# Performance work log

Hardware: AMD Instinct MI355X
Metric: run time of the kernel (lower is better)

The kernel has to match this reference:

```python
import jax, jax.numpy as jnp
import numpy as np

DOWNSAMPLE = 512  # points per cloud, from init_kwargs


def _pairwise_dist(x, y):
    """Batched Euclidean distance matrix. x: (B,n,D), y: (B,m,D) -> (B,n,m)."""
    x2 = jnp.sum(x * x, axis=-1)                     # (B,n)
    y2 = jnp.sum(y * y, axis=-1)                     # (B,m)
    d2 = x2[:, :, None] + y2[:, None, :] - 2.0 * jnp.einsum('bnd,bmd->bnm', x, y)
    pos = d2 > 0.0                                   # guard sqrt(0)/negatives from fp error
    return jnp.where(pos, jnp.sqrt(jnp.where(pos, d2, 1.0)), 0.0)


def setup_inputs() -> dict:
    key = jax.random.key(0)
    k1, k2 = jax.random.split(key)
    inp = jax.random.normal(k1, (65536, 128), dtype=jnp.float32)
    tgt = jax.random.normal(k2, (65536, 128), dtype=jnp.float32)
    return {"input": inp, "target": tgt}


def reference(input, target):
    D = input.shape[-1]
    x = input.reshape(-1, DOWNSAMPLE, D)   # (B, n, D)
    y = target.reshape(-1, DOWNSAMPLE, D)  # (B, n, D)
    # geomloss energy kernel loss with uniform weights:
    # L_b = mean||x-y|| - 0.5*mean||x-x'|| - 0.5*mean||y-y'||
    cross = jnp.mean(_pairwise_dist(x, y), axis=(1, 2))  # (B,)
    xx = jnp.mean(_pairwise_dist(x, x), axis=(1, 2))
    yy = jnp.mean(_pairwise_dist(y, y), axis=(1, 2))
    loss = cross - 0.5 * xx - 0.5 * yy
    return jnp.mean(loss)
```

## Files before the change

kernel.cpp:

```cpp
#include <hip/hip_runtime.h>

typedef __attribute__((ext_vector_type(8))) __bf16 bf16x8;
typedef __attribute__((ext_vector_type(4))) float f32x4;
typedef __attribute__((ext_vector_type(8))) unsigned short ushort8;

#define DSAMP 512
#define DIM   128
#define REG5  16384
#define NPAIR 18

__constant__ unsigned char T_Asrc[NPAIR]  = {0,0,0,0,0,0,0,0, 1,1,1,1,1,1,1,1,1,1};
__constant__ unsigned char T_Ai[NPAIR]    = {0,0,1,1,1,2,2,3, 0,0,0,0,1,1,1,2,2,3};
__constant__ unsigned char T_Bsrc0[NPAIR] = {0,0,0,0,1,0,1,0, 1,1,0,0,1,1,0,1,0,1};
__constant__ unsigned char T_Bsrc1[NPAIR] = {0,0,0,1,1,0,1,1, 1,1,0,0,1,0,0,1,0,0};
__constant__ unsigned char T_Bj0[NPAIR]   = {0,2,1,3,2,2,2,3, 0,2,0,2,1,3,2,2,0,3};
__constant__ unsigned char T_Bj1[NPAIR]   = {1,3,2,1,3,3,3,3, 1,3,1,3,2,0,3,3,3,0};
__constant__ char          T_wc0[NPAIR]   = {2,1,2,1,0,2,0,2, 2,1,0,0,2,1,0,2,0,2};
__constant__ char          T_wc1[NPAIR]   = {1,1,1,0,0,1,0,0, 1,1,0,0,1,0,0,1,0,0};
__constant__ unsigned char T_d0[NPAIR]    = {1,0,1,0,0,1,0,1, 1,0,0,0,1,0,0,1,0,1};

__device__ __forceinline__ ushort8 cvt8(float4 v0, float4 v1, float& ss) {
    ss = v0.x * v0.x + v0.y * v0.y + v0.z * v0.z + v0.w * v0.w
       + v1.x * v1.x + v1.y * v1.y + v1.z * v1.z + v1.w * v1.w;
    ushort8 hv;
    unsigned u;
    u = __float_as_uint(v0.x); hv[0] = (unsigned short)((u + 0x7fffu + ((u >> 16) & 1u)) >> 16);
    u = __float_as_uint(v0.y); hv[1] = (unsigned short)((u + 0x7fffu + ((u >> 16) & 1u)) >> 16);
    u = __float_as_uint(v0.z); hv[2] = (unsigned short)((u + 0x7fffu + ((u >> 16) & 1u)) >> 16);
    u = __float_as_uint(v0.w); hv[3] = (unsigned short)((u + 0x7fffu + ((u >> 16) & 1u)) >> 16);
    u = __float_as_uint(v1.x); hv[4] = (unsigned short)((u + 0x7fffu + ((u >> 16) & 1u)) >> 16);
    u = __float_as_uint(v1.y); hv[5] = (unsigned short)((u + 0x7fffu + ((u >> 16) & 1u)) >> 16);
    u = __float_as_uint(v1.z); hv[6] = (unsigned short)((u + 0x7fffu + ((u >> 16) & 1u)) >> 16);
    u = __float_as_uint(v1.w); hv[7] = (unsigned short)((u + 0x7fffu + ((u >> 16) & 1u)) >> 16);
    return hv;
}

#define LOADB(Bp, cc) do {                                                    \
    const float* gb_ = (Bp) + (size_t)rB * 128 + (cc) * 64 + jbB * 8;         \
    p0 = ((const float4*)gb_)[0];          p1 = ((const float4*)gb_)[1];      \
    p2 = ((const float4*)(gb_ + 4096))[0]; p3 = ((const float4*)(gb_ + 4096))[1]; \
    p4 = ((const float4*)(gb_ + 8192))[0]; p5 = ((const float4*)(gb_ + 8192))[1]; \
    p6 = ((const float4*)(gb_ +12288))[0]; p7 = ((const float4*)(gb_ +12288))[1]; \
} while (0)

#define RED8(sv) do {                       \
    sv += __shfl_down(sv, 4, 8);            \
    sv += __shfl_down(sv, 2, 8);            \
    sv += __shfl_down(sv, 1, 8);            \
} while (0)

#define WRITEB(QnArr, add) do {                                               \
    float ssw_; ushort8 hw_;                                                  \
    hw_ = cvt8(p0, p1, ssw_); *(ushort8*)(dstB +     0) = hw_; RED8(ssw_);    \
    if ((tid & 7) == 0) { if (add) (QnArr)[rB]      += ssw_; else (QnArr)[rB]      = ssw_; } \
    hw_ = cvt8(p2, p3, ssw_); *(ushort8*)(dstB +  4096) = hw_; RED8(ssw_);    \
    if ((tid & 7) == 0) { if (add) (QnArr)[rB + 32] += ssw_; else (QnArr)[rB + 32] = ssw_; } \
    hw_ = cvt8(p4, p5, ssw_); *(ushort8*)(dstB +  8192) = hw_; RED8(ssw_);    \
    if ((tid & 7) == 0) { if (add) (QnArr)[rB + 64] += ssw_; else (QnArr)[rB + 64] = ssw_; } \
    hw_ = cvt8(p6, p7, ssw_); *(ushort8*)(dstB + 12288) = hw_; RED8(ssw_);    \
    if ((tid & 7) == 0) { if (add) (QnArr)[rB + 96] += ssw_; else (QnArr)[rB + 96] = ssw_; } \
} while (0)

__global__ __launch_bounds__(256, 3)
void mmd_fused(const float* __restrict__ x, const float* __restrict__ y,
               float* __restrict__ partials) {
    __shared__ __align__(16) char smem[3 * REG5];
    __shared__ float Pn[128];
    __shared__ float Qn0[128];
    __shared__ float Qn1[128];
    __shared__ float wred[4];

    const int tid = threadIdx.x;
    const int bid = blockIdx.x;
    const int xcd = bid & 7;
    const int seq = bid >> 3;
    const int s   = seq % NPAIR;
    const int grp = seq / NPAIR;
    const int b   = xcd + 8 * grp;

    const int Ai  = T_Ai[s];
    const int Bj0 = T_Bj0[s];
    const int Bj1 = T_Bj1[s];
    const float* Asrc  = T_Asrc[s]  ? y : x;
    const float* B0src = T_Bsrc0[s] ? y : x;
    const float* B1src = T_Bsrc1[s] ? y : x;
    const int wc0 = T_wc0[s], wc1 = T_wc1[s];
    const float w0 = (wc0 == 0) ? 1.0f : ((wc0 == 1) ? -1.0f : -0.5f);
    const float w1 = (wc1 == 0) ? 1.0f : ((wc1 == 1) ? -1.0f : -0.5f);
    const bool dg0 = T_d0[s] != 0;

    const size_t rowbase = (size_t)b * 512;
    const float* Ap  = Asrc  + (rowbase + (size_t)Ai  * 128) * 128;
    const float* Bp0 = B0src + (rowbase + (size_t)Bj0 * 128) * 128;
    const float* Bp1 = B1src + (rowbase + (size_t)Bj1 * 128) * 128;

    const int lane    = tid & 63;
    const int wv      = tid >> 6;
    const int rowHalf = (wv >> 1) * 64;
    const int colHalf = (wv & 1) * 64;
    const int fm      = lane & 15;
    const int kq      = lane >> 4;
    const int sw      = fm & 7;

    const int jbB = tid & 7;
    const int rB  = tid >> 3;
    char* dstB = smem + 2 * REG5 + rB * 128 + ((jbB ^ (rB & 7)) * 16);

    float4 p0, p1, p2, p3, p4, p5, p6, p7;

    f32x4 acc[4][4];
    auto zero_acc = [&]() {
        #pragma unroll
        for (int a2 = 0; a2 < 4; ++a2)
            #pragma unroll
            for (int b2 = 0; b2 < 4; ++b2)
                acc[a2][b2] = (f32x4){0.f, 0.f, 0.f, 0.f};
    };

    auto compute = [&](int creg) {
        const char* Ab = smem + creg * REG5;
        const char* Bb = smem + 2 * REG5;
        #pragma unroll
        for (int ks = 0; ks < 2; ++ks) {
            const int jx = ((ks * 4 + kq) ^ sw) * 16;
            bf16x8 ah[4], bh[4];
            #pragma unroll
            for (int a2 = 0; a2 < 4; ++a2)
                ah[a2] = *(const bf16x8*)(Ab + (rowHalf + a2 * 16 + fm) * 128 + jx);
            #pragma unroll
            for (int b2 = 0; b2 < 4; ++b2)
                bh[b2] = *(const bf16x8*)(Bb + (colHalf + b2 * 16 + fm) * 128 + jx);
            __builtin_amdgcn_s_setprio(1);
            #pragma unroll
            for (int a2 = 0; a2 < 4; ++a2)
                #pragma unroll
                for (int b2 = 0; b2 < 4; ++b2)
                    acc[a2][b2] = __builtin_amdgcn_mfma_f32_16x16x32_bf16(
                        ah[a2], bh[b2], acc[a2][b2], 0, 0, 0);
            __builtin_amdgcn_s_setprio(0);
        }
    };

    auto tile_sum = [&](const float* Qn, bool dg) -> float {
        float Pr[16], Qc[4];
        #pragma unroll
        for (int a2 = 0; a2 < 4; ++a2)
            #pragma unroll
            for (int rg2 = 0; rg2 < 4; ++rg2)
                Pr[a2 * 4 + rg2] = Pn[rowHalf + a2 * 16 + kq * 4 + rg2];
        #pragma unroll
        for (int b2 = 0; b2 < 4; ++b2) Qc[b2] = Qn[colHalf + b2 * 16 + fm];
        float ls = 0.f;
        if (dg) {
            #pragma unroll
            for (int a2 = 0; a2 < 4; ++a2)
                #pragma unroll
                for (int b2 = 0; b2 < 4; ++b2)
                    #pragma unroll
                    for (int rg2 = 0; rg2 < 4; ++rg2) {
                        float d2 = fmaf(-2.0f, acc[a2][b2][rg2], Pr[a2 * 4 + rg2] + Qc[b2]);
                        float v  = __builtin_amdgcn_sqrtf(fmaxf(d2, 0.0f));
                        if ((rowHalf + a2 * 16 + kq * 4 + rg2) == (colHalf + b2 * 16 + fm)) v = 0.f;
                        ls += v;
                    }
        } else {
            #pragma unroll
            for (int a2 = 0; a2 < 4; ++a2)
                #pragma unroll
                for (int b2 = 0; b2 < 4; ++b2)
                    #pragma unroll
                    for (int rg2 = 0; rg2 < 4; ++rg2) {
                        float d2 = fmaf(-2.0f, acc[a2][b2][rg2], Pr[a2 * 4 + rg2] + Qc[b2]);
                        ls += __builtin_amdgcn_sqrtf(fmaxf(d2, 0.0f));
                    }
        }
        return ls;
    };

    LOADB(Bp0, 0);
    #pragma unroll
    for (int it = 0; it < 8; ++it) {
        int u  = it * 256 + tid;
        int jb = u & 7;
        int cc = (u >> 3) & 1;
        int r  = u >> 4;
        const float* g = Ap + (size_t)r * 128 + cc * 64 + jb * 8;
        float4 v0 = ((const float4*)g)[0];
        float4 v1 = ((const float4*)g)[1];
        float ss;
        ushort8 hv = cvt8(v0, v1, ss);
        *(ushort8*)(smem + cc * REG5 + r * 128 + ((jb ^ (r & 7)) * 16)) = hv;
        ss += __shfl_down(ss, 8, 16);
        ss += __shfl_down(ss, 4, 16);
        ss += __shfl_down(ss, 2, 16);
        ss += __shfl_down(ss, 1, 16);
        if ((tid & 15) == 0) Pn[r] = ss;
    }
    WRITEB(Qn0, false);
    __syncthreads();

    zero_acc();
    LOADB(Bp0, 1);
    compute(0);
    __syncthreads();
    WRITEB(Qn0, true);
    __syncthreads();
    LOADB(Bp1, 0);
    compute(1);
    __syncthreads();
    WRITEB(Qn1, false);
    float lsum = w0 * tile_sum(Qn0, dg0);
    zero_acc();
    __syncthreads();

    LOADB(Bp1, 1);
    compute(0);
    __syncthreads();
    WRITEB(Qn1, true);
    __syncthreads();
    compute(1);
    lsum += w1 * tile_sum(Qn1, false);

    #pragma unroll
    for (int off = 32; off > 0; off >>= 1) lsum += __shfl_down(lsum, off, 64);
    if (lane == 0) wred[wv] = lsum;
    __syncthreads();
    if (tid == 0)
        partials[bid] = wred[0] + wred[1] + wred[2] + wred[3];
}

__global__ __launch_bounds__(256, 2)
void mmd_tile_fallback(const float* __restrict__ x, const float* __restrict__ y,
                       float* __restrict__ partials) {
    __shared__ __align__(16) char smem[4 * 128 * 144];
    __shared__ float Pn[128];
    __shared__ float Qn[128];
    __shared__ float wred[4];

    char* Ah = smem;
    char* Al = smem + 1 * 128 * 144;
    char* Bh = smem + 2 * 128 * 144;
    char* Bl = smem + 3 * 128 * 144;

    const int tid  = threadIdx.x;
    const int bid  = blockIdx.x;
    const int tj   = bid & 3;
    const int ti   = (bid >> 2) & 3;
    const int type = (bid >> 4) % 3;
    const int b    = bid / 48;

    const float* Xb = x + (size_t)b * DSAMP * DIM;
    const float* Yb = y + (size_t)b * DSAMP * DIM;
    const float* Pp; const float* Qp; float w;
    if (type == 0)      { Pp = Xb; Qp = Yb; w = 1.0f;  }
    else if (type == 1) { Pp = Xb; Qp = Xb; w = -0.5f; }
    else                { Pp = Yb; Qp = Yb; w = -0.5f; }
    Pp += (size_t)ti * 128 * DIM;
    Qp += (size_t)tj * 128 * DIM;

    {
        const float* rp = (tid < 128) ? (Pp + (size_t)tid * DIM)
                                      : (Qp + (size_t)(tid - 128) * DIM);
        float s = 0.f;
        #pragma unroll
        for (int k4 = 0; k4 < 32; ++k4) {
            float4 v = ((const float4*)rp)[k4];
            s += v.x * v.x + v.y * v.y + v.z * v.z + v.w * v.w;
        }
        if (tid < 128) Pn[tid] = s; else Qn[tid - 128] = s;
    }

    const int lane    = tid & 63;
    const int wv      = tid >> 6;
    const int rowHalf = (wv >> 1) * 64;
    const int colHalf = (wv & 1) * 64;
    const int fm      = lane & 15;
    const int kq      = lane >> 4;

    f32x4 acc[4][4];
    #pragma unroll
    for (int a2 = 0; a2 < 4; ++a2)
        #pragma unroll
        for (int b2 = 0; b2 < 4; ++b2)
            acc[a2][b2] = (f32x4){0.f, 0.f, 0.f, 0.f};

    for (int c = 0; c < 2; ++c) {
        if (c) __syncthreads();
        #pragma unroll
        for (int side = 0; side < 2; ++side) {
            const float* sp = side ? Qp : Pp;
            char* dh = side ? Bh : Ah;
            char* dl = side ? Bl : Al;
            #pragma unroll
            for (int it = 0; it < 4; ++it) {
                int u  = it * 256 + tid;
                int r  = u >> 3;
                int c8 = u & 7;
                const float* g = sp + (size_t)r * DIM + c * 64 + c8 * 8;
                float4 v0 = ((const float4*)g)[0];
                float4 v1 = ((const float4*)g)[1];
                float xs[8] = {v0.x, v0.y, v0.z, v0.w, v1.x, v1.y, v1.z, v1.w};
                ushort8 hv, lv;
                #pragma unroll
                for (int e = 0; e < 8; ++e) {
                    float xv = xs[e];
                    unsigned ub = __float_as_uint(xv);
                    unsigned hr = (ub + 0x7fffu + ((ub >> 16) & 1u)) >> 16;
                    float hf = __uint_as_float(hr << 16);
                    float rs = xv - hf;
                    unsigned ul = __float_as_uint(rs);
                    unsigned lr = (ul + 0x7fffu + ((ul >> 16) & 1u)) >> 16;
                    hv[e] = (unsigned short)hr;
                    lv[e] = (unsigned short)lr;
                }
                *(ushort8*)(dh + r * 144 + c8 * 16) = hv;
                *(ushort8*)(dl + r * 144 + c8 * 16) = lv;
            }
        }
        __syncthreads();
        #pragma unroll
        for (int ks = 0; ks < 2; ++ks) {
            const int kb2 = (ks * 32 + kq * 8) * 2;
            bf16x8 ah[4], al[4], bh[4], bl[4];
            #pragma unroll
            for (int a2 = 0; a2 < 4; ++a2) {
                int ar = rowHalf + a2 * 16 + fm;
                ah[a2] = *(const bf16x8*)(Ah + ar * 144 + kb2);
                al[a2] = *(const bf16x8*)(Al + ar * 144 + kb2);
            }
            #pragma unroll
            for (int b2 = 0; b2 < 4; ++b2) {
                int br = colHalf + b2 * 16 + fm;
                bh[b2] = *(const bf16x8*)(Bh + br * 144 + kb2);
                bl[b2] = *(const bf16x8*)(Bl + br * 144 + kb2);
            }
            #pragma unroll
            for (int a2 = 0; a2 < 4; ++a2)
                #pragma unroll
                for (int b2 = 0; b2 < 4; ++b2) {
                    acc[a2][b2] = __builtin_amdgcn_mfma_f32_16x16x32_bf16(ah[a2], bh[b2], acc[a2][b2], 0, 0, 0);
                    acc[a2][b2] = __builtin_amdgcn_mfma_f32_16x16x32_bf16(ah[a2], bl[b2], acc[a2][b2], 0, 0, 0);
                    acc[a2][b2] = __builtin_amdgcn_mfma_f32_16x16x32_bf16(al[a2], bh[b2], acc[a2][b2], 0, 0, 0);
                }
        }
    }

    const bool selfm = (type != 0) && (ti == tj);
    float lsum = 0.f;
    #pragma unroll
    for (int a2 = 0; a2 < 4; ++a2) {
        int ib = rowHalf + a2 * 16 + kq * 4;
        #pragma unroll
        for (int b2 = 0; b2 < 4; ++b2) {
            int j = colHalf + b2 * 16 + fm;
            float qn = Qn[j];
            #pragma unroll
            for (int rg = 0; rg < 4; ++rg) {
                int i = ib + rg;
                float d2 = Pn[i] + qn - 2.0f * acc[a2][b2][rg];
                if (d2 > 0.f && !(selfm && i == j)) lsum += sqrtf(d2);
            }
        }
    }
    #pragma unroll
    for (int off = 32; off > 0; off >>= 1) lsum += __shfl_down(lsum, off, 64);
    if (lane == 0) wred[wv] = lsum;
    __syncthreads();
    if (tid == 0)
        partials[bid] = (wred[0] + wred[1] + wred[2] + wred[3]) * w;
}

__global__ __launch_bounds__(256)
void mmd_finalize_kernel(const float* __restrict__ partials, int n,
                         float* __restrict__ out, double scale) {
    __shared__ double sh[256];
    double s = 0.0;
    for (int i = threadIdx.x; i < n; i += 256) s += (double)partials[i];
    sh[threadIdx.x] = s;
    __syncthreads();
    for (int off = 128; off > 0; off >>= 1) {
        if ((int)threadIdx.x < off) sh[threadIdx.x] += sh[threadIdx.x + off];
        __syncthreads();
    }
    if (threadIdx.x == 0) out[0] = (float)(sh[0] * scale);
}

extern "C" void kernel_launch(void* const* d_in, const int* in_sizes, int n_in,
                              void* d_out, int out_size, void* d_ws, size_t ws_size,
                              hipStream_t stream) {
    const float* x = (const float*)d_in[0];
    const float* y = (const float*)d_in[1];
    float* out = (float*)d_out;

    const int n = in_sizes[0];
    const int B = n / (DSAMP * DIM);
    const double scale = 1.0 / ((double)B * (double)DSAMP * (double)DSAMP);

    float* partials = (float*)d_ws;
    if (B == 128 && ws_size >= (size_t)(128 * NPAIR) * 4) {
        const int nblocks = 128 * NPAIR;
        mmd_fused<<<dim3(nblocks), dim3(256), 0, stream>>>(x, y, partials);
        mmd_finalize_kernel<<<dim3(1), dim3(256), 0, stream>>>(partials, nblocks, out, scale);
    } else {
        const int nblocks = B * 48;
        mmd_tile_fallback<<<dim3(nblocks), dim3(256), 0, stream>>>(x, y, partials);
        mmd_finalize_kernel<<<dim3(1), dim3(256), 0, stream>>>(partials, nblocks, out, scale);
    }
}
```

Measured before the change: 142.2 us.

## Load B operand straight from global into MFMA registers, skipping LDS staging

Each wave now loads its own B-tile columns from global memory, converts them to bf16 in registers, and feeds them straight to MFMA. Column norms are computed in registers and reduced with cross-lane shuffles. This removes the B shared-memory region, the Qn arrays and most block barriers, and cuts LDS use to two regions, which may allow more blocks per CU. The cost is that waves sharing the same column half load the same B data twice, leaning on the caches, with less coalesced 32-byte-per-lane accesses.

```diff
diff --git a/kernel.cpp b/kernel.cpp
--- a/kernel.cpp
+++ b/kernel.cpp
@@ -35,39 +35,35 @@
     return hv;
 }
 
-#define LOADB(Bp, cc) do {                                                    \
-    const float* gb_ = (Bp) + (size_t)rB * 128 + (cc) * 64 + jbB * 8;         \
-    p0 = ((const float4*)gb_)[0];          p1 = ((const float4*)gb_)[1];      \
-    p2 = ((const float4*)(gb_ + 4096))[0]; p3 = ((const float4*)(gb_ + 4096))[1]; \
-    p4 = ((const float4*)(gb_ + 8192))[0]; p5 = ((const float4*)(gb_ + 8192))[1]; \
-    p6 = ((const float4*)(gb_ +12288))[0]; p7 = ((const float4*)(gb_ +12288))[1]; \
-} while (0)
-
-#define RED8(sv) do {                       \
-    sv += __shfl_down(sv, 4, 8);            \
-    sv += __shfl_down(sv, 2, 8);            \
-    sv += __shfl_down(sv, 1, 8);            \
-} while (0)
-
-#define WRITEB(QnArr, add) do {                                               \
-    float ssw_; ushort8 hw_;                                                  \
-    hw_ = cvt8(p0, p1, ssw_); *(ushort8*)(dstB +     0) = hw_; RED8(ssw_);    \
-    if ((tid & 7) == 0) { if (add) (QnArr)[rB]      += ssw_; else (QnArr)[rB]      = ssw_; } \
-    hw_ = cvt8(p2, p3, ssw_); *(ushort8*)(dstB +  4096) = hw_; RED8(ssw_);    \
-    if ((tid & 7) == 0) { if (add) (QnArr)[rB + 32] += ssw_; else (QnArr)[rB + 32] = ssw_; } \
-    hw_ = cvt8(p4, p5, ssw_); *(ushort8*)(dstB +  8192) = hw_; RED8(ssw_);    \
-    if ((tid & 7) == 0) { if (add) (QnArr)[rB + 64] += ssw_; else (QnArr)[rB + 64] = ssw_; } \
-    hw_ = cvt8(p6, p7, ssw_); *(ushort8*)(dstB + 12288) = hw_; RED8(ssw_);    \
-    if ((tid & 7) == 0) { if (add) (QnArr)[rB + 96] += ssw_; else (QnArr)[rB + 96] = ssw_; } \
+__device__ __forceinline__ bf16x8 cvt8b(float4 v0, float4 v1, float& ss) {
+    ushort8 h = cvt8(v0, v1, ss);
+    return __builtin_bit_cast(bf16x8, h);
+}
+
+#define MFMA16() do {                                                          \
+    acc[0][0] = __builtin_amdgcn_mfma_f32_16x16x32_bf16(ah0, bh0, acc[0][0], 0, 0, 0); \
+    acc[0][1] = __builtin_amdgcn_mfma_f32_16x16x32_bf16(ah0, bh1, acc[0][1], 0, 0, 0); \
+    acc[0][2] = __builtin_amdgcn_mfma_f32_16x16x32_bf16(ah0, bh2, acc[0][2], 0, 0, 0); \
+    acc[0][3] = __builtin_amdgcn_mfma_f32_16x16x32_bf16(ah0, bh3, acc[0][3], 0, 0, 0); \
+    acc[1][0] = __builtin_amdgcn_mfma_f32_16x16x32_bf16(ah1, bh0, acc[1][0], 0, 0, 0); \
+    acc[1][1] = __builtin_amdgcn_mfma_f32_16x16x32_bf16(ah1, bh1, acc[1][1], 0, 0, 0); \
+    acc[1][2] = __builtin_amdgcn_mfma_f32_16x16x32_bf16(ah1, bh2, acc[1][2], 0, 0, 0); \
+    acc[1][3] = __builtin_amdgcn_mfma_f32_16x16x32_bf16(ah1, bh3, acc[1][3], 0, 0, 0); \
+    acc[2][0] = __builtin_amdgcn_mfma_f32_16x16x32_bf16(ah2, bh0, acc[2][0], 0, 0, 0); \
+    acc[2][1] = __builtin_amdgcn_mfma_f32_16x16x32_bf16(ah2, bh1, acc[2][1], 0, 0, 0); \
+    acc[2][2] = __builtin_amdgcn_mfma_f32_16x16x32_bf16(ah2, bh2, acc[2][2], 0, 0, 0); \
+    acc[2][3] = __builtin_amdgcn_mfma_f32_16x16x32_bf16(ah2, bh3, acc[2][3], 0, 0, 0); \
+    acc[3][0] = __builtin_amdgcn_mfma_f32_16x16x32_bf16(ah3, bh0, acc[3][0], 0, 0, 0); \
+    acc[3][1] = __builtin_amdgcn_mfma_f32_16x16x32_bf16(ah3, bh1, acc[3][1], 0, 0, 0); \
+    acc[3][2] = __builtin_amdgcn_mfma_f32_16x16x32_bf16(ah3, bh2, acc[3][2], 0, 0, 0); \
+    acc[3][3] = __builtin_amdgcn_mfma_f32_16x16x32_bf16(ah3, bh3, acc[3][3], 0, 0, 0); \
 } while (0)
 
 __global__ __launch_bounds__(256, 3)
 void mmd_fused(const float* __restrict__ x, const float* __restrict__ y,
                float* __restrict__ partials) {
-    __shared__ __align__(16) char smem[3 * REG5];
+    __shared__ __align__(16) char smem[2 * REG5];
     __shared__ float Pn[128];
-    __shared__ float Qn0[128];
-    __shared__ float Qn1[128];
     __shared__ float wred[4];
 
     const int tid = threadIdx.x;
@@ -102,82 +98,6 @@
     const int kq      = lane >> 4;
     const int sw      = fm & 7;
 
-    const int jbB = tid & 7;
-    const int rB  = tid >> 3;
-    char* dstB = smem + 2 * REG5 + rB * 128 + ((jbB ^ (rB & 7)) * 16);
-
-    float4 p0, p1, p2, p3, p4, p5, p6, p7;
-
-    f32x4 acc[4][4];
-    auto zero_acc = [&]() {
-        #pragma unroll
-        for (int a2 = 0; a2 < 4; ++a2)
-            #pragma unroll
-            for (int b2 = 0; b2 < 4; ++b2)
-                acc[a2][b2] = (f32x4){0.f, 0.f, 0.f, 0.f};
-    };
-
-    auto compute = [&](int creg) {
-        const char* Ab = smem + creg * REG5;
-        const char* Bb = smem + 2 * REG5;
-        #pragma unroll
-        for (int ks = 0; ks < 2; ++ks) {
-            const int jx = ((ks * 4 + kq) ^ sw) * 16;
-            bf16x8 ah[4], bh[4];
-            #pragma unroll
-            for (int a2 = 0; a2 < 4; ++a2)
-                ah[a2] = *(const bf16x8*)(Ab + (rowHalf + a2 * 16 + fm) * 128 + jx);
-            #pragma unroll
-            for (int b2 = 0; b2 < 4; ++b2)
-                bh[b2] = *(const bf16x8*)(Bb + (colHalf + b2 * 16 + fm) * 128 + jx);
-            __builtin_amdgcn_s_setprio(1);
-            #pragma unroll
-            for (int a2 = 0; a2 < 4; ++a2)
-                #pragma unroll
-                for (int b2 = 0; b2 < 4; ++b2)
-                    acc[a2][b2] = __builtin_amdgcn_mfma_f32_16x16x32_bf16(
-                        ah[a2], bh[b2], acc[a2][b2], 0, 0, 0);
-            __builtin_amdgcn_s_setprio(0);
-        }
-    };
-
-    auto tile_sum = [&](const float* Qn, bool dg) -> float {
-        float Pr[16], Qc[4];
-        #pragma unroll
-        for (int a2 = 0; a2 < 4; ++a2)
-            #pragma unroll
-            for (int rg2 = 0; rg2 < 4; ++rg2)
-                Pr[a2 * 4 + rg2] = Pn[rowHalf + a2 * 16 + kq * 4 + rg2];
-        #pragma unroll
-        for (int b2 = 0; b2 < 4; ++b2) Qc[b2] = Qn[colHalf + b2 * 16 + fm];
-        float ls = 0.f;
-        if (dg) {
-            #pragma unroll
-            for (int a2 = 0; a2 < 4; ++a2)
-                #pragma unroll
-                for (int b2 = 0; b2 < 4; ++b2)
-                    #pragma unroll
-                    for (int rg2 = 0; rg2 < 4; ++rg2) {
-                        float d2 = fmaf(-2.0f, acc[a2][b2][rg2], Pr[a2 * 4 + rg2] + Qc[b2]);
-                        float v  = __builtin_amdgcn_sqrtf(fmaxf(d2, 0.0f));
-                        if ((rowHalf + a2 * 16 + kq * 4 + rg2) == (colHalf + b2 * 16 + fm)) v = 0.f;
-                        ls += v;
-                    }
-        } else {
-            #pragma unroll
-            for (int a2 = 0; a2 < 4; ++a2)
-                #pragma unroll
-                for (int b2 = 0; b2 < 4; ++b2)
-                    #pragma unroll
-                    for (int rg2 = 0; rg2 < 4; ++rg2) {
-                        float d2 = fmaf(-2.0f, acc[a2][b2][rg2], Pr[a2 * 4 + rg2] + Qc[b2]);
-                        ls += __builtin_amdgcn_sqrtf(fmaxf(d2, 0.0f));
-                    }
-        }
-        return ls;
-    };
-
-    LOADB(Bp0, 0);
     #pragma unroll
     for (int it = 0; it < 8; ++it) {
         int u  = it * 256 + tid;
@@ -196,30 +116,102 @@
         ss += __shfl_down(ss, 1, 16);
         if ((tid & 15) == 0) Pn[r] = ss;
     }
-    WRITEB(Qn0, false);
     __syncthreads();
 
-    zero_acc();
-    LOADB(Bp0, 1);
-    compute(0);
-    __syncthreads();
-    WRITEB(Qn0, true);
-    __syncthreads();
-    LOADB(Bp1, 0);
-    compute(1);
-    __syncthreads();
-    WRITEB(Qn1, false);
-    float lsum = w0 * tile_sum(Qn0, dg0);
-    zero_acc();
-    __syncthreads();
-
-    LOADB(Bp1, 1);
-    compute(0);
-    __syncthreads();
-    WRITEB(Qn1, true);
-    __syncthreads();
-    compute(1);
-    lsum += w1 * tile_sum(Qn1, false);
+    f32x4 acc[4][4];
+
+    auto tile_pass = [&](const float* Bp, bool dg) -> float {
+        #pragma unroll
+        for (int a2 = 0; a2 < 4; ++a2)
+            #pragma unroll
+            for (int b2 = 0; b2 < 4; ++b2)
+                acc[a2][b2] = (f32x4){0.f, 0.f, 0.f, 0.f};
+        float ssb0 = 0.f, ssb1 = 0.f, ssb2 = 0.f, ssb3 = 0.f;
+        const float* rbase = Bp + (size_t)(colHalf + fm) * DIM + kq * 8;
+        #pragma unroll
+        for (int cc = 0; cc < 2; ++cc) {
+            const char* Ab = smem + cc * REG5;
+            const float* g0 = rbase + cc * 64;
+            float4 qa0 = ((const float4*)(g0       ))[0], qa1 = ((const float4*)(g0       ))[1];
+            float4 qb0 = ((const float4*)(g0 + 2048))[0], qb1 = ((const float4*)(g0 + 2048))[1];
+            float4 qc0 = ((const float4*)(g0 + 4096))[0], qc1 = ((const float4*)(g0 + 4096))[1];
+            float4 qd0 = ((const float4*)(g0 + 6144))[0], qd1 = ((const float4*)(g0 + 6144))[1];
+            float sst;
+            bf16x8 bh0 = cvt8b(qa0, qa1, sst); ssb0 += sst;
+            bf16x8 bh1 = cvt8b(qb0, qb1, sst); ssb1 += sst;
+            bf16x8 bh2 = cvt8b(qc0, qc1, sst); ssb2 += sst;
+            bf16x8 bh3 = cvt8b(qd0, qd1, sst); ssb3 += sst;
+            const float* g1 = g0 + 32;
+            float4 ra0 = ((const float4*)(g1       ))[0], ra1 = ((const float4*)(g1       ))[1];
+            float4 rb0 = ((const float4*)(g1 + 2048))[0], rb1 = ((const float4*)(g1 + 2048))[1];
+            float4 rc0 = ((const float4*)(g1 + 4096))[0], rc1 = ((const float4*)(g1 + 4096))[1];
+            float4 rd0 = ((const float4*)(g1 + 6144))[0], rd1 = ((const float4*)(g1 + 6144))[1];
+            {
+                const int jx0 = (kq ^ sw) * 16;
+                bf16x8 ah0 = *(const bf16x8*)(Ab + (rowHalf +  0 + fm) * 128 + jx0);
+                bf16x8 ah1 = *(const bf16x8*)(Ab + (rowHalf + 16 + fm) * 128 + jx0);
+                bf16x8 ah2 = *(const bf16x8*)(Ab + (rowHalf + 32 + fm) * 128 + jx0);
+                bf16x8 ah3 = *(const bf16x8*)(Ab + (rowHalf + 48 + fm) * 128 + jx0);
+                __builtin_amdgcn_s_setprio(1);
+                MFMA16();
+                __builtin_amdgcn_s_setprio(0);
+            }
+            bh0 = cvt8b(ra0, ra1, sst); ssb0 += sst;
+            bh1 = cvt8b(rb0, rb1, sst); ssb1 += sst;
+            bh2 = cvt8b(rc0, rc1, sst); ssb2 += sst;
+            bh3 = cvt8b(rd0, rd1, sst); ssb3 += sst;
+            {
+                const int jx1 = ((4 + kq) ^ sw) * 16;
+                bf16x8 ah0 = *(const bf16x8*)(Ab + (rowHalf +  0 + fm) * 128 + jx1);
+                bf16x8 ah1 = *(const bf16x8*)(Ab + (rowHalf + 16 + fm) * 128 + jx1);
+                bf16x8 ah2 = *(const bf16x8*)(Ab + (rowHalf + 32 + fm) * 128 + jx1);
+                bf16x8 ah3 = *(const bf16x8*)(Ab + (rowHalf + 48 + fm) * 128 + jx1);
+                __builtin_amdgcn_s_setprio(1);
+                MFMA16();
+                __builtin_amdgcn_s_setprio(0);
+            }
+        }
+        ssb0 += __shfl_xor(ssb0, 16, 64); ssb0 += __shfl_xor(ssb0, 32, 64);
+        ssb1 += __shfl_xor(ssb1, 16, 64); ssb1 += __shfl_xor(ssb1, 32, 64);
+        ssb2 += __shfl_xor(ssb2, 16, 64); ssb2 += __shfl_xor(ssb2, 32, 64);
+        ssb3 += __shfl_xor(ssb3, 16, 64); ssb3 += __shfl_xor(ssb3, 32, 64);
+        float Qc[4] = {ssb0, ssb1, ssb2, ssb3};
+
+        float Pr[16];
+        #pragma unroll
+        for (int a2 = 0; a2 < 4; ++a2)
+            #pragma unroll
+            for (int rg2 = 0; rg2 < 4; ++rg2)
+                Pr[a2 * 4 + rg2] = Pn[rowHalf + a2 * 16 + kq * 4 + rg2];
+        float ls = 0.f;
+        if (dg) {
+            #pragma unroll
+            for (int a2 = 0; a2 < 4; ++a2)
+                #pragma unroll
+                for (int b2 = 0; b2 < 4; ++b2)
+                    #pragma unroll
+                    for (int rg2 = 0; rg2 < 4; ++rg2) {
+                        float d2 = fmaf(-2.0f, acc[a2][b2][rg2], Pr[a2 * 4 + rg2] + Qc[b2]);
+                        float v  = __builtin_amdgcn_sqrtf(fmaxf(d2, 0.0f));
+                        if ((rowHalf + a2 * 16 + kq * 4 + rg2) == (colHalf + b2 * 16 + fm)) v = 0.f;
+                        ls += v;
+                    }
+        } else {
+            #pragma unroll
+            for (int a2 = 0; a2 < 4; ++a2)
+                #pragma unroll
+                for (int b2 = 0; b2 < 4; ++b2)
+                    #pragma unroll
+                    for (int rg2 = 0; rg2 < 4; ++rg2) {
+                        float d2 = fmaf(-2.0f, acc[a2][b2][rg2], Pr[a2 * 4 + rg2] + Qc[b2]);
+                        ls += __builtin_amdgcn_sqrtf(fmaxf(d2, 0.0f));
+                    }
+        }
+        return ls;
+    };
+
+    float lsum = w0 * tile_pass(Bp0, dg0);
+    lsum += w1 * tile_pass(Bp1, false);
 
     #pragma unroll
     for (int off = 32; off > 0; off >>= 1) lsum += __shfl_down(lsum, off, 64);
```

Result: slower. 307.6 us (+116.3%).
